# Kernel optimization log

Measured on AMD Instinct MI355X. Metric: run time of the kernel, lower is better.

The kernel has to match this reference:

```python
import jax, jax.numpy as jnp
import numpy as np

B, C, Hf, Wf, HM, P = 64, 2048, 16, 16, 256, 10  # P = num_parts, NP = graph nodes
NP = P - 1
EPS = 1e-5  # BatchNorm eps

def bn_eval(x, g, b, rm, rv):
    return (x - rm) * jax.lax.rsqrt(rv + EPS) * g + b

def setup_inputs() -> dict:
    key = jax.random.key(0)
    ks = jax.random.split(key, 6)
    return {
        "x_global": jax.random.normal(ks[0], (B, C, Hf, Wf), jnp.float32),
        "x_gcn": jax.random.normal(ks[1], (B, C, Hf, Wf), jnp.float32),
        "mask": jax.random.randint(ks[2], (B, 1, HM, HM), 0, P, jnp.int32),
        "adj": jax.random.uniform(ks[3], (B, NP, NP), jnp.float32),
        "W1": jax.random.normal(ks[4], (C, C), jnp.float32) * 0.02,
        "b1": jnp.zeros((C,), jnp.float32),
        "g1": jnp.ones((NP * C,), jnp.float32), "be1": jnp.zeros((NP * C,), jnp.float32),
        "rm1": jnp.zeros((NP * C,), jnp.float32), "rv1": jnp.ones((NP * C,), jnp.float32),
        "W2": jax.random.normal(ks[5], (C, C), jnp.float32) * 0.02,
        "b2": jnp.zeros((C,), jnp.float32),
        "g2": jnp.ones((NP * C,), jnp.float32), "be2": jnp.zeros((NP * C,), jnp.float32),
        "rm2": jnp.zeros((NP * C,), jnp.float32), "rv2": jnp.ones((NP * C,), jnp.float32),
        "gb_g": jnp.ones((C,), jnp.float32), "gb_b": jnp.zeros((C,), jnp.float32),
        "gb_rm": jnp.zeros((C,), jnp.float32), "gb_rv": jnp.ones((C,), jnp.float32),
        "gn_g": jnp.ones((C,), jnp.float32), "gn_b": jnp.zeros((C,), jnp.float32),
        "gn_rm": jnp.zeros((C,), jnp.float32), "gn_rv": jnp.ones((C,), jnp.float32),
    }

def gc_layer(x, adj, Wt, bias, g, be, rm, rv):
    # GraphConvolution: matmul -> bmm(adj) -> bias -> BN over flattened (B, NP*C)
    s = jnp.einsum('bpc,cd->bpd', x, Wt)
    o = jnp.einsum('bpq,bqd->bpd', adj, s) + bias
    flat = o.reshape(o.shape[0], -1)
    return bn_eval(flat, g, be, rm, rv).reshape(o.shape)

def reference(x_global, x_gcn, mask, adj, W1, b1, g1, be1, rm1, rv1,
              W2, b2, g2, be2, rm2, rv2, gb_g, gb_b, gb_rm, gb_rv,
              gn_g, gn_b, gn_rm, gn_rv):
    # --- global branch: GAP + bottleneck BN (eval) ---
    feat_global = x_global.mean(axis=(2, 3))                      # (B, C)
    bnfeat_global = bn_eval(feat_global, gb_g, gb_b, gb_rm, gb_rv)

    # --- nearest-neighbor downsample of mask to feature-map size ---
    stride = HM // Hf
    mr = mask[:, 0, ::stride, ::stride]                           # (B, h, w)

    # one-hot part masks for classes 1..P-1: (B, h, w, NP)
    onehot = (mr[..., None] == jnp.arange(1, P)).astype(jnp.float32)
    counts = onehot.sum(axis=(1, 2))                              # (B, NP)

    # deterministic part dropout: drop the first present part per image
    drop = jnp.argmax(counts > 0, axis=1) + 1                     # (B,)
    keep = (mr != drop[:, None, None]).astype(jnp.float32)        # (B, h, w)
    x_self = x_gcn * keep[:, None, :, :]

    # segment mean pooling per part: (B, NP, C)
    denom = (counts + 1e-8)[..., None]
    mask_feat = jnp.einsum('bchw,bhwp->bpc', x_gcn, onehot) / denom
    self_feat = jnp.einsum('bchw,bhwp->bpc', x_self, onehot) / denom

    def gcn(x):
        x1 = jax.nn.relu(gc_layer(x, adj, W1, b1, g1, be1, rm1, rv1))
        x2 = jax.nn.relu(gc_layer(x1, adj, W2, b2, g2, be2, rm2, rv2))
        return x2.mean(axis=1), x2.reshape(x2.shape[0], -1)

    feat_gcn, feat_gcn_cat = gcn(mask_feat)
    feat_self, feat_self_cat = gcn(self_feat)
    bnfeat_gcn = bn_eval(feat_gcn, gn_g, gn_b, gn_rm, gn_rv)
    bnfeat_self = bn_eval(feat_self, gn_g, gn_b, gn_rm, gn_rv)

    # concatenate eval-mode outputs into one array: (B, 3*C + 2*NP*C)
    return jnp.concatenate([bnfeat_global, bnfeat_gcn, bnfeat_self,
                            feat_gcn_cat, feat_self_cat], axis=1)
```

## Files before the change

kernel.cpp:

```cpp
#include <hip/hip_runtime.h>
#include <cstdint>
#include <cstddef>

#define EPSV 1e-5f

typedef __bf16 bf16x8 __attribute__((ext_vector_type(8)));
typedef float f32x4 __attribute__((ext_vector_type(4)));

__device__ __forceinline__ unsigned short f2bf(float f) {
  unsigned int u = __float_as_uint(f);
  u += 0x7FFFu + ((u >> 16) & 1u);
  return (unsigned short)(u >> 16);
}

__device__ __forceinline__ void async_copy16(const void* src, void* dst_lds) {
  __builtin_amdgcn_global_load_lds(
      (const __attribute__((address_space(1))) void*)src,
      (__attribute__((address_space(3))) void*)dst_lds, 16, 0, 0);
}

__global__ __launch_bounds__(256) void prep(
    const float* __restrict__ W1, const float* __restrict__ W2,
    unsigned short* __restrict__ Wt1, unsigned short* __restrict__ Wt2,
    const float* __restrict__ xg, const float* __restrict__ gb_g,
    const float* __restrict__ gb_b, const float* __restrict__ gb_rm,
    const float* __restrict__ gb_rv, float* __restrict__ out,
    const int* __restrict__ mask, int* __restrict__ partid,
    float* __restrict__ invden, int* __restrict__ dropm1) {
  int blk = blockIdx.x;
  if (blk < 8192) {
    int z = blk >> 12;
    int rem = blk & 4095;
    int by = rem >> 6, bx = rem & 63;
    const float* W = z ? W2 : W1;
    unsigned short* Wt = z ? Wt2 : Wt1;
    __shared__ float tile[32][33];
    int tx = threadIdx.x & 31;
    int ty = threadIdx.x >> 5;
    int k0 = by * 32, n0 = bx * 32;
#pragma unroll
    for (int i = 0; i < 32; i += 8)
      tile[ty + i][tx] = W[(size_t)(k0 + ty + i) * 2048 + n0 + tx];
    __syncthreads();
#pragma unroll
    for (int i = 0; i < 32; i += 8)
      Wt[(size_t)(n0 + ty + i) * 2048 + k0 + tx] = f2bf(tile[tx][ty + i]);
  } else if (blk < 40960) {
    int gw = (blk - 8192) * 4 + (threadIdx.x >> 6);
    int lane = threadIdx.x & 63;
    float4 v = ((const float4*)(xg + (size_t)gw * 256))[lane];
    float s = v.x + v.y + v.z + v.w;
#pragma unroll
    for (int o = 32; o > 0; o >>= 1) s += __shfl_xor(s, o, 64);
    if (lane == 0) {
      int b = gw >> 11, c = gw & 2047;
      float m = s * (1.f / 256.f);
      out[(size_t)b * 43008 + c] =
          (m - gb_rm[c]) / sqrtf(gb_rv[c] + EPSV) * gb_g[c] + gb_b[c];
    }
  } else {
    int b = blk - 40960;
    int t = threadIdx.x;
    int h = t >> 4, w = t & 15;
    int m = mask[(size_t)b * 65536 + h * 4096 + w * 16];
    partid[b * 256 + t] = m;
    __shared__ int cnt[10];
    if (t < 10) cnt[t] = 0;
    __syncthreads();
    atomicAdd(&cnt[m], 1);
    __syncthreads();
    if (t == 0) {
      int dp = 0;
      for (int p = 8; p >= 0; p--)
        if (cnt[p + 1] > 0) dp = p;
      dropm1[b] = dp;
    }
    if (t < 9) invden[b * 9 + t] = 1.f / ((float)cnt[t + 1] + 1e-8f);
  }
}

__global__ __launch_bounds__(256) void kpool_mfma(
    const float* __restrict__ x, const int* __restrict__ partid,
    const float* __restrict__ invden, const int* __restrict__ dropm1,
    unsigned short* __restrict__ Abuf) {
  __shared__ unsigned short As[64 * 264];
  __shared__ unsigned short Bs[16 * 264];
  __shared__ int pid[256];
  const int t = threadIdx.x;
  const int b = blockIdx.y;
  const int c0 = blockIdx.x * 64;

  pid[t] = partid[b * 256 + t];

  const float4* xgp = (const float4*)(x + ((size_t)(b * 2048 + c0)) * 256);
#pragma unroll
  for (int it = 0; it < 16; it++) {
    int idx = t + it * 256;
    float4 v = xgp[idx];
    int row = idx >> 6, sc = (idx & 63) * 4;
    ushort4 h;
    h.x = f2bf(v.x); h.y = f2bf(v.y); h.z = f2bf(v.z); h.w = f2bf(v.w);
    *(ushort4*)&As[row * 264 + sc] = h;
  }
  __syncthreads();
  {
    int p = t >> 4, s0 = (t & 15) * 16;
#pragma unroll
    for (int j = 0; j < 16; j++)
      Bs[p * 264 + s0 + j] =
          (pid[s0 + j] == p + 1) ? (unsigned short)0x3F80 : (unsigned short)0;
  }
  __syncthreads();

  const int wave = t >> 6;
  const int l16 = t & 15;
  const int quad = (t & 63) >> 4;
  f32x4 acc = (f32x4){0.f, 0.f, 0.f, 0.f};
#pragma unroll
  for (int ks = 0; ks < 8; ks++) {
    bf16x8 a = *(const bf16x8*)&As[(wave * 16 + l16) * 264 + ks * 32 + quad * 8];
    bf16x8 bf = *(const bf16x8*)&Bs[l16 * 264 + ks * 32 + quad * 8];
    acc = __builtin_amdgcn_mfma_f32_16x16x32_bf16(a, bf, acc, 0, 0, 0);
  }

  if (l16 < 9) {
    int p = l16;
    float inv = invden[b * 9 + p];
    int dm1 = dropm1[b];
    int cbase = c0 + wave * 16 + quad * 4;
    ushort4 hm;
    hm.x = f2bf(acc[0] * inv);
    hm.y = f2bf(acc[1] * inv);
    hm.z = f2bf(acc[2] * inv);
    hm.w = f2bf(acc[3] * inv);
    ushort4 hs = (p == dm1) ? (ushort4){0, 0, 0, 0} : hm;
    *(ushort4*)&Abuf[(size_t)(b * 9 + p) * 2048 + cbase] = hm;
    *(ushort4*)&Abuf[(size_t)((64 + b) * 9 + p) * 2048 + cbase] = hs;
  }
}

#define GK 2048
#define SPART (1152 * 2048)
__global__ __launch_bounds__(256) void gemm_db(
    const unsigned short* __restrict__ A, const unsigned short* __restrict__ Bt,
    float* __restrict__ S) {
  __shared__ unsigned short As[2][128 * 64];
  __shared__ unsigned short Bs[2][128 * 64];
  const int tid = threadIdx.x;
  const int lane = tid & 63;
  const int wave = tid >> 6;
  const int wm = (wave >> 1) << 6;
  const int wn = (wave & 1) << 6;
  const int quad = lane >> 4;
  const int l16 = lane & 15;
  const int by = blockIdx.y;
  const int bx = blockIdx.x;
  const int kz = blockIdx.z;

  const unsigned short* Ag = A + (size_t)by * 128 * GK;
  const unsigned short* Bg = Bt + (size_t)bx * 128 * GK;
  S += (size_t)kz * SPART;

  f32x4 acc[4][4];
#pragma unroll
  for (int i = 0; i < 4; i++)
#pragma unroll
    for (int j = 0; j < 4; j++) acc[i][j] = (f32x4){0.f, 0.f, 0.f, 0.f};

  int srow[4], scol[4];
#pragma unroll
  for (int s = 0; s < 4; s++) {
    int idx = tid + s * 256;
    srow[s] = idx >> 3;
    scol[s] = ((idx & 7) ^ (srow[s] & 7)) * 8;
  }

  const int kbeg = kz * 512;

#define STAGE(buf, kk)                                                        \
  do {                                                                        \
    _Pragma("unroll") for (int s = 0; s < 4; s++) {                           \
      int idx = tid + s * 256;                                                \
      async_copy16(Ag + (size_t)srow[s] * GK + (kk) + scol[s],                \
                   &As[buf][idx * 8]);                                        \
    }                                                                         \
    _Pragma("unroll") for (int s = 0; s < 4; s++) {                           \
      int idx = tid + s * 256;                                                \
      async_copy16(Bg + (size_t)srow[s] * GK + (kk) + scol[s],                \
                   &Bs[buf][idx * 8]);                                        \
    }                                                                         \
  } while (0)

  STAGE(0, kbeg);
  asm volatile("s_waitcnt vmcnt(0)" ::: "memory");
  __syncthreads();

  for (int it = 0; it < 8; it++) {
    const int cur = it & 1;
    if (it < 7) STAGE(cur ^ 1, kbeg + (it + 1) * 64);

#pragma unroll
    for (int ks = 0; ks < 2; ks++) {
      bf16x8 af[4], bfr[4];
#pragma unroll
      for (int i = 0; i < 4; i++) {
        int row = wm + i * 16 + l16;
        int slot = row * 8 + ((ks * 4 + quad) ^ (row & 7));
        af[i] = *(const bf16x8*)&As[cur][slot * 8];
      }
#pragma unroll
      for (int j = 0; j < 4; j++) {
        int row = wn + j * 16 + l16;
        int slot = row * 8 + ((ks * 4 + quad) ^ (row & 7));
        bfr[j] = *(const bf16x8*)&Bs[cur][slot * 8];
      }
#pragma unroll
      for (int i = 0; i < 4; i++)
#pragma unroll
        for (int j = 0; j < 4; j++)
          acc[i][j] = __builtin_amdgcn_mfma_f32_16x16x32_bf16(
              af[i], bfr[j], acc[i][j], 0, 0, 0);
    }

    if (it < 7) {
      asm volatile("s_waitcnt vmcnt(0)" ::: "memory");
      __syncthreads();
    }
  }

#pragma unroll
  for (int i = 0; i < 4; i++)
#pragma unroll
    for (int j = 0; j < 4; j++)
#pragma unroll
      for (int r = 0; r < 4; r++) {
        int m = by * 128 + wm + i * 16 + quad * 4 + r;
        int n = bx * 128 + wn + j * 16 + l16;
        S[(size_t)m * 2048 + n] = acc[i][j][r];
      }
}

__global__ __launch_bounds__(256) void epi_mid(
    const float* __restrict__ S, const float* __restrict__ adj,
    const float* __restrict__ bias, const float* __restrict__ g,
    const float* __restrict__ be, const float* __restrict__ rm,
    const float* __restrict__ rv, unsigned short* __restrict__ Aout) {
  int idx = blockIdx.x * 256 + threadIdx.x;
  int d = idx & 2047;
  int bb = idx >> 11;
  int b = bb & 63;
  float s[9];
#pragma unroll
  for (int q = 0; q < 9; q++) {
    size_t off = (size_t)(bb * 9 + q) * 2048 + d;
    s[q] = S[off] + S[off + SPART] + S[off + 2 * SPART] + S[off + 3 * SPART];
  }
#pragma unroll
  for (int p = 0; p < 9; p++) {
    float o = bias[d];
#pragma unroll
    for (int q = 0; q < 9; q++) o += adj[b * 81 + p * 9 + q] * s[q];
    int f = p * 2048 + d;
    float v = (o - rm[f]) / sqrtf(rv[f] + EPSV) * g[f] + be[f];
    v = fmaxf(v, 0.f);
    Aout[(size_t)(bb * 9 + p) * 2048 + d] = f2bf(v);
  }
}

__global__ __launch_bounds__(256) void epi_final(
    const float* __restrict__ S, const float* __restrict__ adj,
    const float* __restrict__ bias, const float* __restrict__ g,
    const float* __restrict__ be, const float* __restrict__ rm,
    const float* __restrict__ rv, const float* __restrict__ gn_g,
    const float* __restrict__ gn_b, const float* __restrict__ gn_rm,
    const float* __restrict__ gn_rv, float* __restrict__ out) {
  int idx = blockIdx.x * 256 + threadIdx.x;
  int d = idx & 2047;
  int bb = idx >> 11;
  int b = bb & 63;
  bool selfb = bb >= 64;
  float s[9];
#pragma unroll
  for (int q = 0; q < 9; q++) {
    size_t off = (size_t)(bb * 9 + q) * 2048 + d;
    s[q] = S[off] + S[off + SPART] + S[off + 2 * SPART] + S[off + 3 * SPART];
  }
  float* orow = out + (size_t)b * 43008;
  size_t catbase = selfb ? 24576 : 6144;
  float mean = 0.f;
#pragma unroll
  for (int p = 0; p < 9; p++) {
    float o = bias[d];
#pragma unroll
    for (int q = 0; q < 9; q++) o += adj[b * 81 + p * 9 + q] * s[q];
    int f = p * 2048 + d;
    float v = (o - rm[f]) / sqrtf(rv[f] + EPSV) * g[f] + be[f];
    v = fmaxf(v, 0.f);
    mean += v;
    orow[catbase + f] = v;
  }
  mean *= (1.f / 9.f);
  orow[(selfb ? 4096 : 2048) + d] =
      (mean - gn_rm[d]) / sqrtf(gn_rv[d] + EPSV) * gn_g[d] + gn_b[d];
}

extern "C" void kernel_launch(void* const* d_in, const int* in_sizes, int n_in,
                              void* d_out, int out_size, void* d_ws,
                              size_t ws_size, hipStream_t stream) {
  const float* x_global = (const float*)d_in[0];
  const float* x_gcn = (const float*)d_in[1];
  const int* mask = (const int*)d_in[2];
  const float* adj = (const float*)d_in[3];
  const float* W1 = (const float*)d_in[4];
  const float* b1 = (const float*)d_in[5];
  const float* g1 = (const float*)d_in[6];
  const float* be1 = (const float*)d_in[7];
  const float* rm1 = (const float*)d_in[8];
  const float* rv1 = (const float*)d_in[9];
  const float* W2 = (const float*)d_in[10];
  const float* b2 = (const float*)d_in[11];
  const float* g2 = (const float*)d_in[12];
  const float* be2 = (const float*)d_in[13];
  const float* rm2 = (const float*)d_in[14];
  const float* rv2 = (const float*)d_in[15];
  const float* gb_g = (const float*)d_in[16];
  const float* gb_b = (const float*)d_in[17];
  const float* gb_rm = (const float*)d_in[18];
  const float* gb_rv = (const float*)d_in[19];
  const float* gn_g = (const float*)d_in[20];
  const float* gn_b = (const float*)d_in[21];
  const float* gn_rm = (const float*)d_in[22];
  const float* gn_rv = (const float*)d_in[23];
  float* out = (float*)d_out;

  char* ws = (char*)d_ws;
  int* partid = (int*)(ws);
  float* invden = (float*)(ws + 65536);
  int* dropm1 = (int*)(ws + 67840);
  unsigned short* Abuf = (unsigned short*)(ws + 131072);
  unsigned short* Wt1 = (unsigned short*)(ws + 4849664);
  unsigned short* Wt2 = (unsigned short*)(ws + 13238272);
  float* S = (float*)(ws + 21626880);

  prep<<<41024, 256, 0, stream>>>(W1, W2, Wt1, Wt2, x_global, gb_g, gb_b,
                                  gb_rm, gb_rv, out, mask, partid, invden,
                                  dropm1);
  kpool_mfma<<<dim3(32, 64), 256, 0, stream>>>(x_gcn, partid, invden, dropm1,
                                               Abuf);
  gemm_db<<<dim3(16, 9, 4), 256, 0, stream>>>(Abuf, Wt1, S);
  epi_mid<<<1024, 256, 0, stream>>>(S, adj, b1, g1, be1, rm1, rv1, Abuf);
  gemm_db<<<dim3(16, 9, 4), 256, 0, stream>>>(Abuf, Wt2, S);
  epi_final<<<1024, 256, 0, stream>>>(S, adj, b2, g2, be2, rm2, rv2, gn_g,
                                      gn_b, gn_rm, gn_rv, out);
}
```

Before: 414.4 us.

## Retile GEMM to 128x64 with split-K 2, precompute BN scale/shift, batch GAP rows

The GEMM tile shrinks from 128x128 to 128x64 and split-K drops from 4 to 2. That keeps the block count while halving partial-sum traffic in the epilogues. The bias and BatchNorm parameters for both graph-conv layers are folded into per-feature scale and shift arrays inside prep, so the epilogues skip the divides and sqrts. The global average pool now reduces four channels per wave and writes a float4. The cost is longer K loops per block and a lower MFMA-to-load ratio on the B tile.

```diff
diff --git a/kernel.cpp b/kernel.cpp
--- a/kernel.cpp
+++ b/kernel.cpp
@@ -26,7 +26,14 @@
     const float* __restrict__ gb_b, const float* __restrict__ gb_rm,
     const float* __restrict__ gb_rv, float* __restrict__ out,
     const int* __restrict__ mask, int* __restrict__ partid,
-    float* __restrict__ invden, int* __restrict__ dropm1) {
+    float* __restrict__ invden, int* __restrict__ dropm1,
+    const float* __restrict__ b1, const float* __restrict__ g1,
+    const float* __restrict__ be1, const float* __restrict__ rm1,
+    const float* __restrict__ rv1, const float* __restrict__ b2,
+    const float* __restrict__ g2, const float* __restrict__ be2,
+    const float* __restrict__ rm2, const float* __restrict__ rv2,
+    float* __restrict__ sc1, float* __restrict__ sh1,
+    float* __restrict__ sc2, float* __restrict__ sh2) {
   int blk = blockIdx.x;
   if (blk < 8192) {
     int z = blk >> 12;
@@ -45,21 +52,38 @@
 #pragma unroll
     for (int i = 0; i < 32; i += 8)
       Wt[(size_t)(n0 + ty + i) * 2048 + k0 + tx] = f2bf(tile[tx][ty + i]);
-  } else if (blk < 40960) {
-    int gw = (blk - 8192) * 4 + (threadIdx.x >> 6);
+  } else if (blk < 16384) {
+    int base = (blk - 8192) * 16 + (threadIdx.x >> 6) * 4;
     int lane = threadIdx.x & 63;
-    float4 v = ((const float4*)(xg + (size_t)gw * 256))[lane];
-    float s = v.x + v.y + v.z + v.w;
-#pragma unroll
-    for (int o = 32; o > 0; o >>= 1) s += __shfl_xor(s, o, 64);
+    const float4* xp = (const float4*)xg + (size_t)base * 64 + lane;
+    float4 v0 = xp[0], v1 = xp[64], v2 = xp[128], v3 = xp[192];
+    float s0 = v0.x + v0.y + v0.z + v0.w;
+    float s1 = v1.x + v1.y + v1.z + v1.w;
+    float s2 = v2.x + v2.y + v2.z + v2.w;
+    float s3 = v3.x + v3.y + v3.z + v3.w;
+#pragma unroll
+    for (int o = 32; o > 0; o >>= 1) {
+      s0 += __shfl_xor(s0, o, 64);
+      s1 += __shfl_xor(s1, o, 64);
+      s2 += __shfl_xor(s2, o, 64);
+      s3 += __shfl_xor(s3, o, 64);
+    }
     if (lane == 0) {
-      int b = gw >> 11, c = gw & 2047;
-      float m = s * (1.f / 256.f);
-      out[(size_t)b * 43008 + c] =
-          (m - gb_rm[c]) / sqrtf(gb_rv[c] + EPSV) * gb_g[c] + gb_b[c];
+      int b = base >> 11, c = base & 2047;
+      float m[4] = {s0 * (1.f / 256.f), s1 * (1.f / 256.f),
+                    s2 * (1.f / 256.f), s3 * (1.f / 256.f)};
+      float4 o4;
+      float* po = &o4.x;
+#pragma unroll
+      for (int r = 0; r < 4; r++) {
+        int cc = c + r;
+        po[r] = (m[r] - gb_rm[cc]) / sqrtf(gb_rv[cc] + EPSV) * gb_g[cc] +
+                gb_b[cc];
+      }
+      *(float4*)(out + (size_t)b * 43008 + c) = o4;
     }
-  } else {
-    int b = blk - 40960;
+  } else if (blk < 16448) {
+    int b = blk - 16384;
     int t = threadIdx.x;
     int h = t >> 4, w = t & 15;
     int m = mask[(size_t)b * 65536 + h * 4096 + w * 16];
@@ -76,6 +100,20 @@
       dropm1[b] = dp;
     }
     if (t < 9) invden[b * 9 + t] = 1.f / ((float)cnt[t + 1] + 1e-8f);
+  } else {
+    int i = (blk - 16448) * 256 + threadIdx.x;
+    int z = i >= 18432;
+    int f = i - z * 18432;
+    int d = f & 2047;
+    const float* g = z ? g2 : g1;
+    const float* be = z ? be2 : be1;
+    const float* rm = z ? rm2 : rm1;
+    const float* rv = z ? rv2 : rv1;
+    const float* bias = z ? b2 : b1;
+    float sc = g[f] / sqrtf(rv[f] + EPSV);
+    float sh = (bias[d] - rm[f]) * sc + be[f];
+    (z ? sc2 : sc1)[f] = sc;
+    (z ? sh2 : sh1)[f] = sh;
   }
 }
 
@@ -145,12 +183,12 @@
     const unsigned short* __restrict__ A, const unsigned short* __restrict__ Bt,
     float* __restrict__ S) {
   __shared__ unsigned short As[2][128 * 64];
-  __shared__ unsigned short Bs[2][128 * 64];
+  __shared__ unsigned short Bs[2][64 * 64];
   const int tid = threadIdx.x;
   const int lane = tid & 63;
   const int wave = tid >> 6;
   const int wm = (wave >> 1) << 6;
-  const int wn = (wave & 1) << 6;
+  const int wn = (wave & 1) << 5;
   const int quad = lane >> 4;
   const int l16 = lane & 15;
   const int by = blockIdx.y;
@@ -158,35 +196,42 @@
   const int kz = blockIdx.z;
 
   const unsigned short* Ag = A + (size_t)by * 128 * GK;
-  const unsigned short* Bg = Bt + (size_t)bx * 128 * GK;
+  const unsigned short* Bg = Bt + (size_t)bx * 64 * GK;
   S += (size_t)kz * SPART;
 
-  f32x4 acc[4][4];
+  f32x4 acc[4][2];
 #pragma unroll
   for (int i = 0; i < 4; i++)
 #pragma unroll
-    for (int j = 0; j < 4; j++) acc[i][j] = (f32x4){0.f, 0.f, 0.f, 0.f};
-
-  int srow[4], scol[4];
+    for (int j = 0; j < 2; j++) acc[i][j] = (f32x4){0.f, 0.f, 0.f, 0.f};
+
+  int srA[4], scA[4];
 #pragma unroll
   for (int s = 0; s < 4; s++) {
     int idx = tid + s * 256;
-    srow[s] = idx >> 3;
-    scol[s] = ((idx & 7) ^ (srow[s] & 7)) * 8;
-  }
-
-  const int kbeg = kz * 512;
+    srA[s] = idx >> 3;
+    scA[s] = ((idx & 7) ^ (srA[s] & 7)) * 8;
+  }
+  int srB[2], scB[2];
+#pragma unroll
+  for (int s = 0; s < 2; s++) {
+    int idx = tid + s * 256;
+    srB[s] = idx >> 3;
+    scB[s] = ((idx & 7) ^ (srB[s] & 7)) * 8;
+  }
+
+  const int kbeg = kz * 1024;
 
 #define STAGE(buf, kk)                                                        \
   do {                                                                        \
     _Pragma("unroll") for (int s = 0; s < 4; s++) {                           \
       int idx = tid + s * 256;                                                \
-      async_copy16(Ag + (size_t)srow[s] * GK + (kk) + scol[s],                \
+      async_copy16(Ag + (size_t)srA[s] * GK + (kk) + scA[s],                  \
                    &As[buf][idx * 8]);                                        \
     }                                                                         \
-    _Pragma("unroll") for (int s = 0; s < 4; s++) {                           \
+    _Pragma("unroll") for (int s = 0; s < 2; s++) {                           \
       int idx = tid + s * 256;                                                \
-      async_copy16(Bg + (size_t)srow[s] * GK + (kk) + scol[s],                \
+      async_copy16(Bg + (size_t)srB[s] * GK + (kk) + scB[s],                  \
                    &Bs[buf][idx * 8]);                                        \
     }                                                                         \
   } while (0)
@@ -195,13 +240,13 @@
   asm volatile("s_waitcnt vmcnt(0)" ::: "memory");
   __syncthreads();
 
-  for (int it = 0; it < 8; it++) {
+  for (int it = 0; it < 16; it++) {
     const int cur = it & 1;
-    if (it < 7) STAGE(cur ^ 1, kbeg + (it + 1) * 64);
+    if (it < 15) STAGE(cur ^ 1, kbeg + (it + 1) * 64);
 
 #pragma unroll
     for (int ks = 0; ks < 2; ks++) {
-      bf16x8 af[4], bfr[4];
+      bf16x8 af[4], bfr[2];
 #pragma unroll
       for (int i = 0; i < 4; i++) {
         int row = wm + i * 16 + l16;
@@ -209,7 +254,7 @@
         af[i] = *(const bf16x8*)&As[cur][slot * 8];
       }
 #pragma unroll
-      for (int j = 0; j < 4; j++) {
+      for (int j = 0; j < 2; j++) {
         int row = wn + j * 16 + l16;
         int slot = row * 8 + ((ks * 4 + quad) ^ (row & 7));
         bfr[j] = *(const bf16x8*)&Bs[cur][slot * 8];
@@ -217,12 +262,12 @@
 #pragma unroll
       for (int i = 0; i < 4; i++)
 #pragma unroll
-        for (int j = 0; j < 4; j++)
+        for (int j = 0; j < 2; j++)
           acc[i][j] = __builtin_amdgcn_mfma_f32_16x16x32_bf16(
               af[i], bfr[j], acc[i][j], 0, 0, 0);
     }
 
-    if (it < 7) {
+    if (it < 15) {
       asm volatile("s_waitcnt vmcnt(0)" ::: "memory");
       __syncthreads();
     }
@@ -231,20 +276,19 @@
 #pragma unroll
   for (int i = 0; i < 4; i++)
 #pragma unroll
-    for (int j = 0; j < 4; j++)
+    for (int j = 0; j < 2; j++)
 #pragma unroll
       for (int r = 0; r < 4; r++) {
         int m = by * 128 + wm + i * 16 + quad * 4 + r;
-        int n = bx * 128 + wn + j * 16 + l16;
+        int n = bx * 64 + wn + j * 16 + l16;
         S[(size_t)m * 2048 + n] = acc[i][j][r];
       }
 }
 
 __global__ __launch_bounds__(256) void epi_mid(
     const float* __restrict__ S, const float* __restrict__ adj,
-    const float* __restrict__ bias, const float* __restrict__ g,
-    const float* __restrict__ be, const float* __restrict__ rm,
-    const float* __restrict__ rv, unsigned short* __restrict__ Aout) {
+    const float* __restrict__ sc, const float* __restrict__ sh,
+    unsigned short* __restrict__ Aout) {
   int idx = blockIdx.x * 256 + threadIdx.x;
   int d = idx & 2047;
   int bb = idx >> 11;
@@ -253,27 +297,25 @@
 #pragma unroll
   for (int q = 0; q < 9; q++) {
     size_t off = (size_t)(bb * 9 + q) * 2048 + d;
-    s[q] = S[off] + S[off + SPART] + S[off + 2 * SPART] + S[off + 3 * SPART];
+    s[q] = S[off] + S[off + SPART];
   }
 #pragma unroll
   for (int p = 0; p < 9; p++) {
-    float o = bias[d];
+    float o = 0.f;
 #pragma unroll
     for (int q = 0; q < 9; q++) o += adj[b * 81 + p * 9 + q] * s[q];
     int f = p * 2048 + d;
-    float v = (o - rm[f]) / sqrtf(rv[f] + EPSV) * g[f] + be[f];
-    v = fmaxf(v, 0.f);
+    float v = fmaxf(o * sc[f] + sh[f], 0.f);
     Aout[(size_t)(bb * 9 + p) * 2048 + d] = f2bf(v);
   }
 }
 
 __global__ __launch_bounds__(256) void epi_final(
     const float* __restrict__ S, const float* __restrict__ adj,
-    const float* __restrict__ bias, const float* __restrict__ g,
-    const float* __restrict__ be, const float* __restrict__ rm,
-    const float* __restrict__ rv, const float* __restrict__ gn_g,
-    const float* __restrict__ gn_b, const float* __restrict__ gn_rm,
-    const float* __restrict__ gn_rv, float* __restrict__ out) {
+    const float* __restrict__ sc, const float* __restrict__ sh,
+    const float* __restrict__ gn_g, const float* __restrict__ gn_b,
+    const float* __restrict__ gn_rm, const float* __restrict__ gn_rv,
+    float* __restrict__ out) {
   int idx = blockIdx.x * 256 + threadIdx.x;
   int d = idx & 2047;
   int bb = idx >> 11;
@@ -283,19 +325,18 @@
 #pragma unroll
   for (int q = 0; q < 9; q++) {
     size_t off = (size_t)(bb * 9 + q) * 2048 + d;
-    s[q] = S[off] + S[off + SPART] + S[off + 2 * SPART] + S[off + 3 * SPART];
+    s[q] = S[off] + S[off + SPART];
   }
   float* orow = out + (size_t)b * 43008;
   size_t catbase = selfb ? 24576 : 6144;
   float mean = 0.f;
 #pragma unroll
   for (int p = 0; p < 9; p++) {
-    float o = bias[d];
+    float o = 0.f;
 #pragma unroll
     for (int q = 0; q < 9; q++) o += adj[b * 81 + p * 9 + q] * s[q];
     int f = p * 2048 + d;
-    float v = (o - rm[f]) / sqrtf(rv[f] + EPSV) * g[f] + be[f];
-    v = fmaxf(v, 0.f);
+    float v = fmaxf(o * sc[f] + sh[f], 0.f);
     mean += v;
     orow[catbase + f] = v;
   }
@@ -341,15 +382,20 @@
   unsigned short* Wt1 = (unsigned short*)(ws + 4849664);
   unsigned short* Wt2 = (unsigned short*)(ws + 13238272);
   float* S = (float*)(ws + 21626880);
-
-  prep<<<41024, 256, 0, stream>>>(W1, W2, Wt1, Wt2, x_global, gb_g, gb_b,
+  float* sc1 = (float*)(ws + 40501248);
+  float* sh1 = (float*)(ws + 40574976);
+  float* sc2 = (float*)(ws + 40648704);
+  float* sh2 = (float*)(ws + 40722432);
+
+  prep<<<16592, 256, 0, stream>>>(W1, W2, Wt1, Wt2, x_global, gb_g, gb_b,
                                   gb_rm, gb_rv, out, mask, partid, invden,
-                                  dropm1);
+                                  dropm1, b1, g1, be1, rm1, rv1, b2, g2, be2,
+                                  rm2, rv2, sc1, sh1, sc2, sh2);
   kpool_mfma<<<dim3(32, 64), 256, 0, stream>>>(x_gcn, partid, invden, dropm1,
                                                Abuf);
-  gemm_db<<<dim3(16, 9, 4), 256, 0, stream>>>(Abuf, Wt1, S);
-  epi_mid<<<1024, 256, 0, stream>>>(S, adj, b1, g1, be1, rm1, rv1, Abuf);
-  gemm_db<<<dim3(16, 9, 4), 256, 0, stream>>>(Abuf, Wt2, S);
-  epi_final<<<1024, 256, 0, stream>>>(S, adj, b2, g2, be2, rm2, rv2, gn_g,
-                                      gn_b, gn_rm, gn_rv, out);
-}
+  gemm_db<<<dim3(32, 9, 2), 256, 0, stream>>>(Abuf, Wt1, S);
+  epi_mid<<<1024, 256, 0, stream>>>(S, adj, sc1, sh1, Abuf);
+  gemm_db<<<dim3(32, 9, 2), 256, 0, stream>>>(Abuf, Wt2, S);
+  epi_final<<<1024, 256, 0, stream>>>(S, adj, sc2, sh2, gn_g, gn_b, gn_rm,
+                                      gn_rv, out);
+}
```

Measured after the change: 407.3 us. About the same (-1.7%).
